# Kernel optimization log

Hardware: AMD Instinct MI355X
Metric: run time of the kernel (lower is better)

## Reference

```python
import jax, jax.numpy as jnp
import numpy as np

N = 50000       # num_nodes
R = 32          # num_relations
H = 16          # hidden channels
C = 8           # num_classes
E = 1_600_000   # num_edges (avg degree 32)


def setup_inputs() -> dict:
    key = jax.random.key(0)
    ks = jax.random.split(key, 8)
    edge_index = jax.random.randint(ks[0], (2, E), 0, N, dtype=jnp.int64)
    edge_type = jnp.sort(jax.random.randint(ks[1], (E,), 0, R, dtype=jnp.int64))
    s1 = 1.0 / np.sqrt(N)
    s2 = 1.0 / np.sqrt(H)
    return {
        "edge_index": edge_index,
        "edge_type": edge_type,
        "weight1": jax.random.normal(ks[2], (R, N, H), jnp.float32) * s1,
        "root1": jax.random.normal(ks[3], (N, H), jnp.float32) * s1,
        "bias1": jnp.zeros((H,), jnp.float32),
        "weight2": jax.random.normal(ks[4], (R, H, C), jnp.float32) * s2,
        "root2": jax.random.normal(ks[5], (H, C), jnp.float32) * s2,
        "bias2": jnp.zeros((C,), jnp.float32),
    }


def reference(edge_index, edge_type, weight1, root1, bias1, weight2, root2, bias2):
    # R-GCN with mean aggregation per relation (PyG RGCNConv semantics).
    src, dst = edge_index[0], edge_index[1]
    # combined segment id: one segment per (relation, dst node)
    seg = edge_type * N + dst  # [E]
    ones = jnp.ones((E,), weight1.dtype)
    cnt = jax.ops.segment_sum(ones, seg, num_segments=R * N)          # [R*N]
    denom = jnp.maximum(cnt, 1.0)[:, None]

    # ---- layer 1: x = None -> identity features; message_r(j) = weight1[r, j] ----
    msg1 = weight1[edge_type, src]                                     # [E, H] gather
    mean1 = jax.ops.segment_sum(msg1, seg, num_segments=R * N) / denom # [R*N, H]
    h = mean1.reshape(R, N, H).sum(0) + root1 + bias1                  # [N, H]
    h = jax.nn.relu(h)

    # ---- layer 2: aggregate features per relation, then relation-specific GEMM ----
    msg2 = h[src]                                                       # [E, H]
    mean2 = jax.ops.segment_sum(msg2, seg, num_segments=R * N) / denom  # [R*N, H]
    mean2 = mean2.reshape(R, N, H)
    out = jnp.einsum('rnf,rfo->no', mean2, weight2) + h @ root2 + bias2 # [N, C]
    return jax.nn.log_softmax(out, axis=1)
```

## Files before the change

### kernel.cpp

```cpp
#include <hip/hip_runtime.h>
#include <math.h>

#define NN 50000
#define RR 32
#define HH 16
#define CC 8
#define SHIFT 6
#define BSZ 64
#define NB 782
#define G 256
#define BINS (BSZ * RR)
#define STAGE_MAX 4096


__global__ void hist_k(const int* __restrict__ dst, int* __restrict__ hist, int E) {
    __shared__ int lh[NB];
    int g = blockIdx.x, tid = threadIdx.x;
    for (int j = tid; j < NB; j += 256) lh[j] = 0;
    __syncthreads();
    int chunk = (E + G - 1) / G;
    int beg = g * chunk, end = min(beg + chunk, E);
    for (int i = beg + tid; i < end; i += 256)
        atomicAdd(&lh[dst[i] >> SHIFT], 1);
    __syncthreads();
    for (int j = tid; j < NB; j += 256) hist[g * NB + j] = lh[j];
}

__global__ void scanA_k(const int* __restrict__ hist, int* __restrict__ btot) {
    __shared__ int red[4];
    int b = blockIdx.x, t = threadIdx.x;
    int v = hist[t * NB + b];
#pragma unroll
    for (int m = 1; m < 64; m <<= 1) v += __shfl_xor(v, m);
    if ((t & 63) == 0) red[t >> 6] = v;
    __syncthreads();
    if (t == 0) btot[b] = red[0] + red[1] + red[2] + red[3];
}

__global__ void scanB_k(const int* __restrict__ btot, int* __restrict__ boff) {
    __shared__ int lds[1024];
    int t = threadIdx.x;
    int v = (t < NB) ? btot[t] : 0;
    lds[t] = v;
    __syncthreads();
    for (int ofs = 1; ofs < 1024; ofs <<= 1) {
        int add = (t >= ofs) ? lds[t - ofs] : 0;
        __syncthreads();
        lds[t] += add;
        __syncthreads();
    }
    if (t < NB) boff[t] = lds[t] - v;
    if (t == NB - 1) boff[NB] = lds[t];
}

__global__ void scanC_k(const int* __restrict__ hist, const int* __restrict__ boff,
                        int* __restrict__ pos) {
    __shared__ int lds[256];
    int b = blockIdx.x, t = threadIdx.x;
    int v = hist[t * NB + b];
    lds[t] = v;
    __syncthreads();
    for (int ofs = 1; ofs < 256; ofs <<= 1) {
        int add = (t >= ofs) ? lds[t - ofs] : 0;
        __syncthreads();
        lds[t] += add;
        __syncthreads();
    }
    pos[t * NB + b] = boff[b] + lds[t] - v;
}

__global__ void scatter2_k(const int* __restrict__ src, const int* __restrict__ dst,
                           const int* __restrict__ et, const int* __restrict__ pos,
                           unsigned* __restrict__ bucket, int E) {
    __shared__ int cur[NB];
    int g = blockIdx.x, tid = threadIdx.x;
    for (int j = tid; j < NB; j += 256) cur[j] = pos[g * NB + j];
    __syncthreads();
    int chunk = (E + G - 1) / G;
    int beg = g * chunk, end = min(beg + chunk, E);
    for (int i = beg + tid; i < end; i += 256) {
        int d = dst[i];
        int p = atomicAdd(&cur[d >> SHIFT], 1);
        bucket[p] = (unsigned)src[i] | ((unsigned)et[i] << 16) |
                    ((unsigned)(d & (BSZ - 1)) << 21);
    }
}


__global__ __launch_bounds__(256) void sortfin_k(
        const unsigned* __restrict__ bucket, const int* __restrict__ boff,
        unsigned* __restrict__ sorted, int* __restrict__ off, float* __restrict__ inv) {
    __shared__ int bins[BINS];
    __shared__ unsigned stage[STAGE_MAX];
    __shared__ int ts[256];
    int b = blockIdx.x, t = threadIdx.x;
    int e0 = boff[b], n = boff[b + 1] - e0;
    int d0 = b * BSZ;
    int ndst = NN - d0; if (ndst > BSZ) ndst = BSZ;
    for (int j = t; j < BINS; j += 256) bins[j] = 0;
    __syncthreads();
    for (int i = t; i < n; i += 256) {
        unsigned rec = bucket[e0 + i];
        int key = ((rec >> 21) & 63) * RR + ((rec >> 16) & 31);
        atomicAdd(&bins[key], 1);
    }
    __syncthreads();
    for (int j = t; j < ndst * RR; j += 256)
        inv[d0 * RR + j] = 1.0f / fmaxf((float)bins[j], 1.0f);
    int loc[8]; int s = 0;
#pragma unroll
    for (int k = 0; k < 8; ++k) { loc[k] = bins[t * 8 + k]; s += loc[k]; }
    ts[t] = s;
    __syncthreads();
    for (int ofs = 1; ofs < 256; ofs <<= 1) {
        int add = (t >= ofs) ? ts[t - ofs] : 0;
        __syncthreads();
        ts[t] += add;
        __syncthreads();
    }
    int run = ts[t] - s;
    __syncthreads();
#pragma unroll
    for (int k = 0; k < 8; ++k) { int c = loc[k]; bins[t * 8 + k] = run; run += c; }
    __syncthreads();
    for (int dl = t; dl < ndst; dl += 256) off[d0 + dl] = e0 + bins[dl * RR];
    if (b == NB - 1 && t == 0) off[NN] = e0 + n;
    __syncthreads();
    if (n <= STAGE_MAX) {
        for (int i = t; i < n; i += 256) {
            unsigned rec = bucket[e0 + i];
            int key = ((rec >> 21) & 63) * RR + ((rec >> 16) & 31);
            int p = atomicAdd(&bins[key], 1);
            stage[p] = rec & 0x1FFFFF;
        }
        __syncthreads();
        for (int i = t; i < n; i += 256) sorted[e0 + i] = stage[i];
    } else {
        for (int i = t; i < n; i += 256) {
            unsigned rec = bucket[e0 + i];
            int key = ((rec >> 21) & 63) * RR + ((rec >> 16) & 31);
            int p = atomicAdd(&bins[key], 1);
            sorted[e0 + p] = rec & 0x1FFFFF;
        }
    }
}


__global__ __launch_bounds__(256) void layer1_k(
        const unsigned* __restrict__ sorted, const int* __restrict__ off,
        const float* __restrict__ inv, const float4* __restrict__ w1v,
        const float4* __restrict__ root1v, const float4* __restrict__ bias1v,
        float4* __restrict__ hv) {
    int d = (blockIdx.x * blockDim.x + threadIdx.x) >> 6;
    if (d >= NN) return;
    int lane = threadIdx.x & 63;
    int q = lane & 3;
    int b0 = off[d], b1 = off[d + 1];
    float4 acc = make_float4(0.f, 0.f, 0.f, 0.f);
    for (int i = b0 + (lane >> 2); i < b1; i += 16) {
        unsigned rec = sorted[i];
        int s = rec & 0xFFFF, r = (rec >> 16) & 31;
        float sc = inv[d * RR + r];
        float4 w = w1v[(size_t)(r * NN + s) * 4 + q];
        acc.x += w.x * sc; acc.y += w.y * sc; acc.z += w.z * sc; acc.w += w.w * sc;
    }
#pragma unroll
    for (int m = 4; m < 64; m <<= 1) {
        acc.x += __shfl_xor(acc.x, m); acc.y += __shfl_xor(acc.y, m);
        acc.z += __shfl_xor(acc.z, m); acc.w += __shfl_xor(acc.w, m);
    }
    if (lane < 4) {
        float4 rt = root1v[d * 4 + lane];
        float4 bs = bias1v[lane];
        float4 o;
        o.x = fmaxf(acc.x + rt.x + bs.x, 0.f);
        o.y = fmaxf(acc.y + rt.y + bs.y, 0.f);
        o.z = fmaxf(acc.z + rt.z + bs.z, 0.f);
        o.w = fmaxf(acc.w + rt.w + bs.w, 0.f);
        hv[d * 4 + lane] = o;
    }
}


__global__ __launch_bounds__(256) void layer2_k(
        const unsigned* __restrict__ sorted, const int* __restrict__ off,
        const float* __restrict__ inv, const float* __restrict__ h,
        const float* __restrict__ w2, const float* __restrict__ root2,
        const float* __restrict__ bias2, float* __restrict__ out) {
    int d = (blockIdx.x * blockDim.x + threadIdx.x) >> 6;
    if (d >= NN) return;
    int lane = threadIdx.x & 63;
    int sub = lane >> 4, f = lane & 15;
    int b0 = off[d], b1 = off[d + 1];
    float4 alo = make_float4(0.f, 0.f, 0.f, 0.f);
    float4 ahi = make_float4(0.f, 0.f, 0.f, 0.f);
    for (int i = b0 + sub; i < b1; i += 4) {
        unsigned rec = sorted[i];
        int s = rec & 0xFFFF, r = (rec >> 16) & 31;
        float p = h[s * HH + f] * inv[d * RR + r];
        const float4* w = (const float4*)(w2 + (r * HH + f) * CC);
        float4 wlo = w[0], whi = w[1];
        alo.x += p * wlo.x; alo.y += p * wlo.y; alo.z += p * wlo.z; alo.w += p * wlo.w;
        ahi.x += p * whi.x; ahi.y += p * whi.y; ahi.z += p * whi.z; ahi.w += p * whi.w;
    }
#pragma unroll
    for (int m = 1; m < 64; m <<= 1) {
        alo.x += __shfl_xor(alo.x, m); alo.y += __shfl_xor(alo.y, m);
        alo.z += __shfl_xor(alo.z, m); alo.w += __shfl_xor(alo.w, m);
        ahi.x += __shfl_xor(ahi.x, m); ahi.y += __shfl_xor(ahi.y, m);
        ahi.z += __shfl_xor(ahi.z, m); ahi.w += __shfl_xor(ahi.w, m);
    }
    if (lane == 0) {
        float v[CC] = {alo.x, alo.y, alo.z, alo.w, ahi.x, ahi.y, ahi.z, ahi.w};
        float hd[HH];
        const float4* hvp = (const float4*)(h + d * HH);
#pragma unroll
        for (int k = 0; k < 4; ++k) {
            float4 t4 = hvp[k];
            hd[k * 4 + 0] = t4.x; hd[k * 4 + 1] = t4.y;
            hd[k * 4 + 2] = t4.z; hd[k * 4 + 3] = t4.w;
        }
#pragma unroll
        for (int c = 0; c < CC; ++c) v[c] += bias2[c];
#pragma unroll
        for (int ff = 0; ff < HH; ++ff) {
            float hf = hd[ff];
#pragma unroll
            for (int c = 0; c < CC; ++c) v[c] += hf * root2[ff * CC + c];
        }
        float m0 = v[0];
#pragma unroll
        for (int c = 1; c < CC; ++c) m0 = fmaxf(m0, v[c]);
        float ssum = 0.f;
#pragma unroll
        for (int c = 0; c < CC; ++c) ssum += expf(v[c] - m0);
        float z = m0 + logf(ssum);
        float4* ov = (float4*)(out + d * CC);
        ov[0] = make_float4(v[0] - z, v[1] - z, v[2] - z, v[3] - z);
        ov[1] = make_float4(v[4] - z, v[5] - z, v[6] - z, v[7] - z);
    }
}


extern "C" void kernel_launch(void* const* d_in, const int* in_sizes, int n_in,
                              void* d_out, int out_size, void* d_ws, size_t ws_size,
                              hipStream_t stream) {
    const int*   edge_index = (const int*)d_in[0];
    const int*   edge_type  = (const int*)d_in[1];
    const float* weight1    = (const float*)d_in[2];
    const float* root1      = (const float*)d_in[3];
    const float* bias1      = (const float*)d_in[4];
    const float* weight2    = (const float*)d_in[5];
    const float* root2      = (const float*)d_in[6];
    const float* bias2      = (const float*)d_in[7];
    float* out = (float*)d_out;

    const int E = in_sizes[1];
    const int* src = edge_index;
    const int* dst = edge_index + E;

    char* p = (char*)d_ws;
    auto alloc = [&](size_t bytes) -> void* {
        void* r = (void*)p; p += (bytes + 255) & ~(size_t)255; return r;
    };
    int*      hist   = (int*)     alloc(sizeof(int) * (size_t)G * NB);
    int*      pos    = (int*)     alloc(sizeof(int) * (size_t)G * NB);
    int*      btot   = (int*)     alloc(sizeof(int) * NB);
    int*      boff   = (int*)     alloc(sizeof(int) * (NB + 1));
    int*      off    = (int*)     alloc(sizeof(int) * (NN + 1));
    unsigned* bucket = (unsigned*)alloc(sizeof(unsigned) * (size_t)E);
    unsigned* sorted = (unsigned*)alloc(sizeof(unsigned) * (size_t)E);
    float*    inv    = (float*)   alloc(sizeof(float) * (size_t)NN * RR);
    float*    h      = (float*)   alloc(sizeof(float) * (size_t)NN * HH);
    (void)ws_size;

    hist_k<<<G, 256, 0, stream>>>(dst, hist, E);
    scanA_k<<<NB, 256, 0, stream>>>(hist, btot);
    scanB_k<<<1, 1024, 0, stream>>>(btot, boff);
    scanC_k<<<NB, 256, 0, stream>>>(hist, boff, pos);
    scatter2_k<<<G, 256, 0, stream>>>(src, dst, edge_type, pos, bucket, E);
    sortfin_k<<<NB, 256, 0, stream>>>(bucket, boff, sorted, off, inv);

    int nblk = (NN * 64 + 255) / 256;
    layer1_k<<<nblk, 256, 0, stream>>>(sorted, off, inv, (const float4*)weight1,
                                       (const float4*)root1, (const float4*)bias1,
                                       (float4*)h);
    layer2_k<<<nblk, 256, 0, stream>>>(sorted, off, inv, h, weight2, root2,
                                       bias2, out);
}
```

Before: 148.0 us.

## Precompute per-node relation projections h·W2 before layer-2 aggregation

Adds a kernel that computes hw[s, r, :] = h[s] @ weight2[r] for every node and relation. Layer 2 then gathers 8-wide projected values per edge instead of gathering 16 features and doing a 16x8 GEMV per edge, so the per-edge FMA work and reductions shrink. The cost is writing and then randomly reading a 51 MB intermediate (N*R*C floats), and each edge gather now touches a scattered 32-byte segment.

Measured after the change: 148.9 us. About the same (+0.6%).

```diff
diff --git a/kernel.cpp b/kernel.cpp
--- a/kernel.cpp
+++ b/kernel.cpp
@@ -11,6 +11,7 @@
 #define G 256
 #define BINS (BSZ * RR)
 #define STAGE_MAX 4096
+#define SCH 64
 
 
 __global__ void hist_k(const int* __restrict__ dst, int* __restrict__ hist, int E) {
@@ -182,62 +183,71 @@
 }
 
 
+__global__ __launch_bounds__(256) void hwbuild_k(
+        const float* __restrict__ h, const float* __restrict__ w2,
+        float* __restrict__ hw) {
+    __shared__ float4 hs[SCH * 4];
+    int tid = threadIdx.x;
+    int r = tid >> 3, c = tid & 7;
+    float4 w0, w1, w2r, w3;
+    {
+        const float* wb = w2 + (r * HH) * CC + c;
+        w0 = make_float4(wb[0*CC], wb[1*CC], wb[2*CC], wb[3*CC]);
+        w1 = make_float4(wb[4*CC], wb[5*CC], wb[6*CC], wb[7*CC]);
+        w2r = make_float4(wb[8*CC], wb[9*CC], wb[10*CC], wb[11*CC]);
+        w3 = make_float4(wb[12*CC], wb[13*CC], wb[14*CC], wb[15*CC]);
+    }
+    int s0 = blockIdx.x * SCH;
+    int nnodes = NN - s0; if (nnodes > SCH) nnodes = SCH;
+    const float4* hg = (const float4*)(h + s0 * HH);
+    for (int j = tid; j < nnodes * 4; j += 256) hs[j] = hg[j];
+    __syncthreads();
+    for (int sl = 0; sl < nnodes; ++sl) {
+        float4 h0 = hs[sl * 4 + 0], h1 = hs[sl * 4 + 1];
+        float4 h2 = hs[sl * 4 + 2], h3 = hs[sl * 4 + 3];
+        float acc = h0.x * w0.x + h0.y * w0.y + h0.z * w0.z + h0.w * w0.w
+                  + h1.x * w1.x + h1.y * w1.y + h1.z * w1.z + h1.w * w1.w
+                  + h2.x * w2r.x + h2.y * w2r.y + h2.z * w2r.z + h2.w * w2r.w
+                  + h3.x * w3.x + h3.y * w3.y + h3.z * w3.z + h3.w * w3.w;
+        hw[(size_t)(s0 + sl) * (RR * CC) + tid] = acc;
+    }
+}
+
+
 __global__ __launch_bounds__(256) void layer2_k(
         const unsigned* __restrict__ sorted, const int* __restrict__ off,
-        const float* __restrict__ inv, const float* __restrict__ h,
-        const float* __restrict__ w2, const float* __restrict__ root2,
+        const float* __restrict__ inv, const float* __restrict__ hw,
+        const float* __restrict__ h, const float* __restrict__ root2,
         const float* __restrict__ bias2, float* __restrict__ out) {
     int d = (blockIdx.x * blockDim.x + threadIdx.x) >> 6;
     if (d >= NN) return;
     int lane = threadIdx.x & 63;
-    int sub = lane >> 4, f = lane & 15;
+    int sub = lane >> 3, c = lane & 7;
     int b0 = off[d], b1 = off[d + 1];
-    float4 alo = make_float4(0.f, 0.f, 0.f, 0.f);
-    float4 ahi = make_float4(0.f, 0.f, 0.f, 0.f);
-    for (int i = b0 + sub; i < b1; i += 4) {
+    float acc = 0.f;
+    for (int i = b0 + sub; i < b1; i += 8) {
         unsigned rec = sorted[i];
         int s = rec & 0xFFFF, r = (rec >> 16) & 31;
-        float p = h[s * HH + f] * inv[d * RR + r];
-        const float4* w = (const float4*)(w2 + (r * HH + f) * CC);
-        float4 wlo = w[0], whi = w[1];
-        alo.x += p * wlo.x; alo.y += p * wlo.y; alo.z += p * wlo.z; alo.w += p * wlo.w;
-        ahi.x += p * whi.x; ahi.y += p * whi.y; ahi.z += p * whi.z; ahi.w += p * whi.w;
-    }
-#pragma unroll
-    for (int m = 1; m < 64; m <<= 1) {
-        alo.x += __shfl_xor(alo.x, m); alo.y += __shfl_xor(alo.y, m);
-        alo.z += __shfl_xor(alo.z, m); alo.w += __shfl_xor(alo.w, m);
-        ahi.x += __shfl_xor(ahi.x, m); ahi.y += __shfl_xor(ahi.y, m);
-        ahi.z += __shfl_xor(ahi.z, m); ahi.w += __shfl_xor(ahi.w, m);
-    }
-    if (lane == 0) {
-        float v[CC] = {alo.x, alo.y, alo.z, alo.w, ahi.x, ahi.y, ahi.z, ahi.w};
-        float hd[HH];
-        const float4* hvp = (const float4*)(h + d * HH);
-#pragma unroll
-        for (int k = 0; k < 4; ++k) {
-            float4 t4 = hvp[k];
-            hd[k * 4 + 0] = t4.x; hd[k * 4 + 1] = t4.y;
-            hd[k * 4 + 2] = t4.z; hd[k * 4 + 3] = t4.w;
-        }
-#pragma unroll
-        for (int c = 0; c < CC; ++c) v[c] += bias2[c];
-#pragma unroll
-        for (int ff = 0; ff < HH; ++ff) {
-            float hf = hd[ff];
-#pragma unroll
-            for (int c = 0; c < CC; ++c) v[c] += hf * root2[ff * CC + c];
-        }
-        float m0 = v[0];
-#pragma unroll
-        for (int c = 1; c < CC; ++c) m0 = fmaxf(m0, v[c]);
-        float ssum = 0.f;
-#pragma unroll
-        for (int c = 0; c < CC; ++c) ssum += expf(v[c] - m0);
-        float z = m0 + logf(ssum);
-        float4* ov = (float4*)(out + d * CC);
-        ov[0] = make_float4(v[0] - z, v[1] - z, v[2] - z, v[3] - z);
-        ov[1] = make_float4(v[4] - z, v[5] - z, v[6] - z, v[7] - z);
+        acc += hw[(size_t)s * (RR * CC) + r * CC + c] * inv[d * RR + r];
+    }
+    acc += __shfl_xor(acc, 8);
+    acc += __shfl_xor(acc, 16);
+    acc += __shfl_xor(acc, 32);
+    if (lane < 8) {
+        float v = acc + bias2[c];
+        const float* hd = h + d * HH;
+#pragma unroll
+        for (int f = 0; f < HH; ++f) v += hd[f] * root2[f * CC + c];
+        float m = v;
+        m = fmaxf(m, __shfl_xor(m, 1));
+        m = fmaxf(m, __shfl_xor(m, 2));
+        m = fmaxf(m, __shfl_xor(m, 4));
+        float ex = expf(v - m);
+        float ssum = ex;
+        ssum += __shfl_xor(ssum, 1);
+        ssum += __shfl_xor(ssum, 2);
+        ssum += __shfl_xor(ssum, 4);
+        out[d * CC + c] = v - m - logf(ssum);
     }
 }
 
@@ -272,6 +282,7 @@
     unsigned* sorted = (unsigned*)alloc(sizeof(unsigned) * (size_t)E);
     float*    inv    = (float*)   alloc(sizeof(float) * (size_t)NN * RR);
     float*    h      = (float*)   alloc(sizeof(float) * (size_t)NN * HH);
+    float*    hw     = (float*)   alloc(sizeof(float) * (size_t)NN * RR * CC);
     (void)ws_size;
 
     hist_k<<<G, 256, 0, stream>>>(dst, hist, E);
@@ -285,6 +296,6 @@
     layer1_k<<<nblk, 256, 0, stream>>>(sorted, off, inv, (const float4*)weight1,
                                        (const float4*)root1, (const float4*)bias1,
                                        (float4*)h);
-    layer2_k<<<nblk, 256, 0, stream>>>(sorted, off, inv, h, weight2, root2,
-                                       bias2, out);
-}
+    hwbuild_k<<<(NN + SCH - 1) / SCH, 256, 0, stream>>>(h, weight2, hw);
+    layer2_k<<<nblk, 256, 0, stream>>>(sorted, off, inv, hw, h, root2, bias2, out);
+}
```
